# Optimization experiments

Hardware: AMD Instinct MI355X
Metric: run time of the kernel (lower is better)

The kernel has to match this reference:

```python
import jax, jax.numpy as jnp
import numpy as np

B, S, D, H, DK, DFF, L = 4, 1024, 1024, 16, 64, 4096, 128

def setup_inputs() -> dict:
    key = jax.random.key(0)
    ks = jax.random.split(key, 20)
    stdv = 1.0 / np.sqrt(D)
    u = lambda k, shape, s=stdv: jax.random.uniform(k, shape, jnp.float32, -s, s)
    x = jax.random.normal(ks[0], (B, S, D), jnp.float32)
    causal = jnp.triu(jnp.ones((S, S), bool), 1)          # True = masked
    attn_mask = jnp.broadcast_to(causal, (B, S, S))
    return {
        "x": x,
        "attn_mask": attn_mask,
        "W_q": u(ks[1], (H * DK, D)), "b_q": jnp.zeros((H * DK,)),
        "W_k": u(ks[2], (H * DK, D)), "b_k": jnp.zeros((H * DK,)),
        "W_v": u(ks[3], (H * DK, D)), "b_v": jnp.zeros((H * DK,)),
        "W_o": u(ks[4], (D, H * DK)), "b_o": jnp.zeros((D,)),
        "W_rel": u(ks[5], (2 * L + 1, DK), 1.0 / np.sqrt(DK)),
        "ln1_alpha": jnp.ones((D,)), "ln1_bias": jnp.zeros((D,)),
        "ln2_alpha": jnp.ones((D,)), "ln2_bias": jnp.zeros((D,)),
        "W1": u(ks[6], (DFF, D)), "b1": jnp.zeros((DFF,)),
        "W2": u(ks[7], (D, DFF)), "b2": jnp.zeros((D,)),
    }

def _layer_norm(x, alpha, bias, eps=1e-5):
    # Faithful to source: (x - mean) / (std + eps), std is biased (unbiased=False)
    m = jnp.mean(x, axis=-1, keepdims=True)
    std = jnp.sqrt(jnp.mean((x - m) ** 2, axis=-1, keepdims=True))
    return alpha * (x - m) / (std + eps) + bias

def reference(x, attn_mask, W_q, b_q, W_k, b_k, W_v, b_v, W_o, b_o, W_rel,
              ln1_alpha, ln1_bias, ln2_alpha, ln2_bias, W1, b1, W2, b2):
    b, s, d = x.shape
    q = (x @ W_q.T + b_q).reshape(b, s, H, DK)
    k = (x @ W_k.T + b_k).reshape(b, s, H, DK)
    v = (x @ W_v.T + b_v).reshape(b, s, H, DK)
    # relative position bias table lookup -> [s, s, DK]
    idx = jnp.clip(jnp.arange(s)[:, None] - jnp.arange(s)[None, :], -L, L) + L
    pos = W_rel[idx]
    # NOTE: original uses rel_pos_k_emb for BOTH pos_key and pos_value (as in source).
    scores = jnp.einsum('bqnd,bknd->bnqk', q, k) + jnp.einsum('bqnd,qkd->bnqk', q, pos)
    scores = scores / np.sqrt(DK)
    scores = jnp.where(attn_mask[:, None, :, :], jnp.float32(-10000.0), scores)
    attn = jax.nn.softmax(scores, axis=-1)
    out = jnp.einsum('bnqk,bknd->bnqd', attn, v) + jnp.einsum('bnqk,qkd->bnqd', attn, pos)
    out = out.transpose(0, 2, 1, 3).reshape(b, s, H * DK)
    out = out @ W_o.T + b_o
    # post-LN transformer layer: LN(x + attn), then LN(h + FFN(h))
    h = _layer_norm(x + out, ln1_alpha, ln1_bias)
    f = jax.nn.relu(h @ W1.T + b1) @ W2.T + b2
    return _layer_norm(h + f, ln2_alpha, ln2_bias)
```

## Files before the change

### kernel.cpp

```cpp
#include <hip/hip_runtime.h>
#include <cmath>
#include <cstdint>

typedef __bf16 bf16;
typedef __bf16 bf16x8 __attribute__((ext_vector_type(8)));
typedef __bf16 bf16x4 __attribute__((ext_vector_type(4)));
typedef float f32x4 __attribute__((ext_vector_type(4)));

__device__ __forceinline__ void async_ld16(const void* g, void* l) {
  __builtin_amdgcn_global_load_lds(
      (__attribute__((address_space(1))) void*)(uintptr_t)g,
      (__attribute__((address_space(3))) void*)l, 16, 0, 0);
}

__global__ __launch_bounds__(256) void cast_all(
    const float* __restrict__ x,  const float* __restrict__ wq, const float* __restrict__ wk,
    const float* __restrict__ wv, const float* __restrict__ wo, const float* __restrict__ w1,
    const float* __restrict__ w2,
    bf16* xb, bf16* wqb, bf16* wkb, bf16* wvb, bf16* wob, bf16* w1b, bf16* w2b)
{
  int i = blockIdx.x * 256 + threadIdx.x;
  const int M1 = 1 << 20, Q = 1 << 18;
  const float* src; bf16* dst; int off;
  if      (i < M1)            { src = x;  dst = xb;  off = i; }
  else if (i < M1 + Q)        { src = wq; dst = wqb; off = i - M1; }
  else if (i < M1 + 2 * Q)    { src = wk; dst = wkb; off = i - M1 - Q; }
  else if (i < M1 + 3 * Q)    { src = wv; dst = wvb; off = i - M1 - 2 * Q; }
  else if (i < M1 + 4 * Q)    { src = wo; dst = wob; off = i - M1 - 3 * Q; }
  else if (i < 3 * M1)        { src = w1; dst = w1b; off = i - M1 - 4 * Q; }
  else                        { src = w2; dst = w2b; off = i - 3 * M1; }
  float4 v = ((const float4*)src)[off];
  bf16x4 o; o[0]=(bf16)v.x; o[1]=(bf16)v.y; o[2]=(bf16)v.z; o[3]=(bf16)v.w;
  ((bf16x4*)dst)[off] = o;
}

template<int BM>
__device__ __forceinline__ void gemm_core(
    const bf16* __restrict__ A, const bf16* __restrict__ Bm, const float* __restrict__ bias,
    float* __restrict__ outF, bf16* __restrict__ outB,
    const float* __restrict__ residF, const bf16* __restrict__ residB,
    int N, int kld, int kbeg, int kend, int relu, bf16* As, bf16* Bs)
{
  constexpr int MI = BM / 32;
  const int tid  = threadIdx.x;
  const int wave = tid >> 6, lane = tid & 63;
  const int lr = lane & 15, lq = lane >> 4;
  const int bm = blockIdx.x * BM, bn = blockIdx.y * 128;
  const int wm = (wave >> 1) * (BM / 2), wn = (wave & 1) * 64;
  const int srow = lane >> 2, scol = (lane & 3) * 8;

  const f32x4 fz = {0.f, 0.f, 0.f, 0.f};
  f32x4 acc[MI][4];
#pragma unroll
  for (int i = 0; i < MI; i++)
#pragma unroll
    for (int j = 0; j < 4; j++) acc[i][j] = fz;

  for (int k0 = kbeg; k0 < kend; k0 += 32) {
    __syncthreads();
    if (BM == 128) {
#pragma unroll
      for (int cc = 0; cc < 2; ++cc) {
        int c = wave * 2 + cc;
        async_ld16(A + (size_t)(bm + c * 16 + srow) * kld + k0 + scol, As + c * 512);
      }
    } else {
      async_ld16(A + (size_t)(bm + wave * 16 + srow) * kld + k0 + scol, As + wave * 512);
    }
#pragma unroll
    for (int cc = 0; cc < 2; ++cc) {
      int c = wave * 2 + cc;
      async_ld16(Bm + (size_t)(bn + c * 16 + srow) * kld + k0 + scol, Bs + c * 512);
    }
    __syncthreads();
    bf16x8 af[MI], bfr[4];
#pragma unroll
    for (int mi = 0; mi < MI; mi++) af[mi]  = *(const bf16x8*)(As + (wm + mi*16 + lr)*32 + lq*8);
#pragma unroll
    for (int ni = 0; ni < 4; ni++) bfr[ni] = *(const bf16x8*)(Bs + (wn + ni*16 + lr)*32 + lq*8);
#pragma unroll
    for (int mi = 0; mi < MI; mi++)
#pragma unroll
      for (int ni = 0; ni < 4; ni++)
        acc[mi][ni] = __builtin_amdgcn_mfma_f32_16x16x32_bf16(af[mi], bfr[ni], acc[mi][ni], 0, 0, 0);
  }

#pragma unroll
  for (int ni = 0; ni < 4; ni++) {
    int n = bn + wn + ni*16 + lr;
    float bv = bias ? bias[n] : 0.0f;
#pragma unroll
    for (int mi = 0; mi < MI; mi++) {
#pragma unroll
      for (int r = 0; r < 4; r++) {
        int m = bm + wm + mi*16 + lq*4 + r;
        size_t idx = (size_t)m * N + n;
        float v = acc[mi][ni][r] + bv;
        if (relu) v = fmaxf(v, 0.0f);
        if (residF) v += residF[idx];
        if (residB) v += (float)residB[idx];
        if (outF) outF[idx] = v;
        else      outB[idx] = (bf16)v;
      }
    }
  }
}

template<int BM>
__global__ __launch_bounds__(256) void gemm_bt(
    const bf16* A, const bf16* Bm, const float* bias,
    float* outF, bf16* outB, const float* residF, const bf16* residB,
    int N, int K, int relu)
{
  __shared__ bf16 As[BM * 32];
  __shared__ bf16 Bs[128 * 32];
  gemm_core<BM>(A, Bm, bias, outF, outB, residF, residB, N, K, 0, K, relu, As, Bs);
}

__global__ __launch_bounds__(256) void gemm_splitk(
    const bf16* A, const bf16* Bm, float* part, int N, int kld, int kchunk)
{
  __shared__ bf16 As[128 * 32];
  __shared__ bf16 Bs[128 * 32];
  const int z = blockIdx.z;
  gemm_core<128>(A, Bm, nullptr, part + (size_t)z * 4096 * N, nullptr, nullptr, nullptr,
                 N, kld, z * kchunk, (z + 1) * kchunk, 0, As, Bs);
}

__global__ __launch_bounds__(256) void gemm_qkv(
    const bf16* A, const bf16* Bq, const bf16* Bk, const bf16* Bv,
    const float* bq, const float* bk, const float* bv,
    bf16* Oq, bf16* Ok, bf16* Ov, int N, int K)
{
  __shared__ bf16 As[128 * 32];
  __shared__ bf16 Bs[128 * 32];
  const bf16* Bm  = blockIdx.z == 0 ? Bq : (blockIdx.z == 1 ? Bk : Bv);
  const float* bi = blockIdx.z == 0 ? bq : (blockIdx.z == 1 ? bk : bv);
  bf16* O         = blockIdx.z == 0 ? Oq : (blockIdx.z == 1 ? Ok : Ov);
  gemm_core<128>(A, Bm, bi, nullptr, O, nullptr, nullptr, N, K, 0, K, 0, As, Bs);
}

#define S_LEN 1024
#define ROWSTR 1024

__global__ __launch_bounds__(256, 3) void attn_kernel(
    const bf16* __restrict__ Qg, const bf16* __restrict__ Kg, const bf16* __restrict__ Vg,
    const float* __restrict__ Wrel, bf16* __restrict__ Og)
{
  __shared__ __align__(16) bf16 hist[64][136];
  __shared__ __align__(16) bf16 rel_s[64][132];
  __shared__ __align__(16) bf16 vtp[9216];
  bf16* V_T  = vtp;
  bf16* Pb   = vtp + 4608;
  bf16* Wst  = vtp;
  bf16* Wr_t = vtp;
  float* lbuf = (float*)rel_s;
  float* hbuf = lbuf + 256;

  const int tid = threadIdx.x;
  const int wave = tid >> 6, lane = tid & 63;
  const int lr = lane & 15, lq = lane >> 4;
  const int qblk = 15 - blockIdx.x;
  const int b = blockIdx.y >> 4, h = blockIdx.y & 15;
  const int q0 = qblk * 64;
  const int T = qblk + 1;
  const int nearStart = (T > 3) ? T - 3 : 0;
  const size_t rowbase = (size_t)b * S_LEN * ROWSTR + h * 64;
  const f32x4 fz = {0.f, 0.f, 0.f, 0.f};

  for (int e = tid; e < 128 * 64; e += 256) {
    int t = e >> 6, d = e & 63;
    Wst[t * 72 + d] = (bf16)Wrel[(size_t)(128 + t) * 64 + d];
  }
  for (int e = tid; e < 64 * 68; e += 256) ((uint*)hist)[e] = 0u;

  bf16x8 qf[4][2];
#pragma unroll
  for (int qt = 0; qt < 4; qt++)
#pragma unroll
    for (int c = 0; c < 2; c++)
      qf[qt][c] = *(const bf16x8*)(Qg + rowbase + (size_t)(q0 + qt*16 + lr) * ROWSTR + c*32 + lq*8);

  bf16x8 wb[2];
#pragma unroll
  for (int c = 0; c < 2; c++)
#pragma unroll
    for (int j = 0; j < 8; j++)
      wb[c][j] = (bf16)Wrel[(size_t)256 * 64 + c*32 + lq*8 + j];

  __syncthreads();

#pragma unroll
  for (int tt = 0; tt < 2; ++tt)
#pragma unroll
    for (int qt = 0; qt < 4; ++qt) {
      f32x4 a = fz;
#pragma unroll
      for (int c = 0; c < 2; c++) {
        bf16x8 wf = *(const bf16x8*)(Wst + (wave*32 + tt*16 + lr) * 72 + c*32 + lq*8);
        a = __builtin_amdgcn_mfma_f32_16x16x32_bf16(wf, qf[qt][c], a, 0, 0, 0);
      }
      bf16x4 pk; pk[0]=(bf16)a[0]; pk[1]=(bf16)a[1]; pk[2]=(bf16)a[2]; pk[3]=(bf16)a[3];
      *(bf16x4*)(&rel_s[qt*16 + lr][wave*32 + tt*16 + lq*4]) = pk;
    }
  {
    f32x4 a = fz;
#pragma unroll
    for (int c = 0; c < 2; c++)
      a = __builtin_amdgcn_mfma_f32_16x16x32_bf16(wb[c], qf[wave][c], a, 0, 0, 0);
    if (lq == 0) rel_s[wave*16 + lr][128] = (bf16)a[0];
  }
  __syncthreads();

  float relc[4];
#pragma unroll
  for (int qt = 0; qt < 4; qt++) relc[qt] = 0.125f * (float)rel_s[qt*16 + lr][128];

  float l_p[4] = {0.f,0.f,0.f,0.f}, h_p[4] = {0.f,0.f,0.f,0.f};
  f32x4 acc_o[4];
#pragma unroll
  for (int dt = 0; dt < 4; dt++) acc_o[dt] = fz;

  const int vrow = 2 * (tid >> 3);
  const int vcol = (tid & 7) * 8;
  const int krow = 16 * wave + lr;

  uint4 va, vb, va2, vb2;
  bf16x8 kf0, kf1, kn0, kn1;
  {
    const bf16* vp = Vg + rowbase + (size_t)vrow * ROWSTR + vcol;
    va = *(const uint4*)vp; vb = *(const uint4*)(vp + ROWSTR);
    const bf16* kp = Kg + rowbase + (size_t)krow * ROWSTR + lq*8;
    kf0 = *(const bf16x8*)kp; kf1 = *(const bf16x8*)(kp + 32);
  }

  for (int kt = 0; kt < T; ++kt) {
    const int k0 = kt * 64;

    f32x4 sc[4];
#pragma unroll
    for (int qt = 0; qt < 4; qt++) {
      sc[qt] = __builtin_amdgcn_mfma_f32_16x16x32_bf16(kf0, qf[qt][0], fz, 0, 0, 0);
      sc[qt] = __builtin_amdgcn_mfma_f32_16x16x32_bf16(kf1, qf[qt][1], sc[qt], 0, 0, 0);
    }
    if (kt + 1 < T) {
      const bf16* vp = Vg + rowbase + (size_t)(k0 + 64 + vrow) * ROWSTR + vcol;
      va2 = *(const uint4*)vp; vb2 = *(const uint4*)(vp + ROWSTR);
      const bf16* kp = Kg + rowbase + (size_t)(k0 + 64 + krow) * ROWSTR + lq*8;
      kn0 = *(const bf16x8*)kp; kn1 = *(const bf16x8*)(kp + 32);
    }

    float pw[4][4];
    if (kt < nearStart) {
#pragma unroll
      for (int qt = 0; qt < 4; qt++) {
#pragma unroll
        for (int r = 0; r < 4; r++) pw[qt][r] = __expf(fmaf(sc[qt][r], 0.125f, relc[qt]));
        float s4 = pw[qt][0] + pw[qt][1] + pw[qt][2] + pw[qt][3];
        l_p[qt] += s4; h_p[qt] += s4;
      }
    } else {
#pragma unroll
      for (int qt = 0; qt < 4; qt++) {
        int qg = q0 + qt*16 + lr;
#pragma unroll
        for (int r = 0; r < 4; r++) {
          int kg = k0 + 16*wave + lq*4 + r;
          float p = 0.0f;
          if (kg <= qg) {
            int t = qg - kg; int tc = t > 128 ? 128 : t;
            p = __expf((sc[qt][r] + (float)rel_s[qt*16 + lr][tc]) * 0.125f);
            l_p[qt] += p;
            if (t >= 128) h_p[qt] += p;
            else          hist[qt*16 + lr][t] = (bf16)p;
          }
          pw[qt][r] = p;
        }
      }
    }

    __syncthreads();
    {
      const ushort* pa = (const ushort*)&va;
      const ushort* pb = (const ushort*)&vb;
#pragma unroll
      for (int j = 0; j < 8; j++) {
        uint w = (uint)pa[j] | ((uint)pb[j] << 16);
        *(uint*)(V_T + (vcol + j) * 72 + vrow) = w;
      }
    }
#pragma unroll
    for (int qt = 0; qt < 4; qt++) {
      bf16x4 pk; pk[0]=(bf16)pw[qt][0]; pk[1]=(bf16)pw[qt][1];
                 pk[2]=(bf16)pw[qt][2]; pk[3]=(bf16)pw[qt][3];
      *(bf16x4*)(Pb + (qt*16 + lr) * 72 + 16*wave + lq*4) = pk;
    }
    __syncthreads();

#pragma unroll
    for (int c = 0; c < 2; c++) {
      bf16x8 pf = *(const bf16x8*)(Pb + (16*wave + lr) * 72 + c*32 + lq*8);
#pragma unroll
      for (int dt = 0; dt < 4; dt++) {
        bf16x8 vf = *(const bf16x8*)(V_T + (dt*16 + lr) * 72 + c*32 + lq*8);
        acc_o[dt] = __builtin_amdgcn_mfma_f32_16x16x32_bf16(pf, vf, acc_o[dt], 0, 0, 0);
      }
    }
    kf0 = kn0; kf1 = kn1; va = va2; vb = vb2;
  }

#pragma unroll
  for (int qt = 0; qt < 4; qt++) {
    l_p[qt] += __shfl_xor(l_p[qt], 16); l_p[qt] += __shfl_xor(l_p[qt], 32);
    h_p[qt] += __shfl_xor(h_p[qt], 16); h_p[qt] += __shfl_xor(h_p[qt], 32);
  }
  __syncthreads();
  if (lq == 0) {
#pragma unroll
    for (int qt = 0; qt < 4; qt++) {
      lbuf[wave*64 + qt*16 + lr] = l_p[qt];
      hbuf[wave*64 + qt*16 + lr] = h_p[qt];
    }
  }
  for (int e = tid; e < 64 * 128; e += 256) {
    int d = e >> 7, t = e & 127;
    Wr_t[d * 136 + t] = (bf16)Wrel[(size_t)(128 + t) * 64 + d];
  }
  __syncthreads();
#pragma unroll
  for (int c = 0; c < 4; c++) {
    bf16x8 hf = *(const bf16x8*)&hist[wave*16 + lr][c*32 + lq*8];
#pragma unroll
    for (int dt = 0; dt < 4; dt++) {
      bf16x8 wf = *(const bf16x8*)(Wr_t + (dt*16 + lr) * 136 + c*32 + lq*8);
      acc_o[dt] = __builtin_amdgcn_mfma_f32_16x16x32_bf16(hf, wf, acc_o[dt], 0, 0, 0);
    }
  }
  float l4[4], h4[4];
#pragma unroll
  for (int r = 0; r < 4; r++) {
    int q = wave*16 + lq*4 + r;
    l4[r] = lbuf[q] + lbuf[64+q] + lbuf[128+q] + lbuf[192+q];
    h4[r] = hbuf[q] + hbuf[64+q] + hbuf[128+q] + hbuf[192+q];
  }
#pragma unroll
  for (int dt = 0; dt < 4; dt++) {
    float wv = Wrel[(size_t)256 * 64 + dt*16 + lr];
#pragma unroll
    for (int r = 0; r < 4; r++) acc_o[dt][r] += h4[r] * wv;
  }
#pragma unroll
  for (int dt = 0; dt < 4; dt++)
#pragma unroll
    for (int r = 0; r < 4; r++) {
      int qg = q0 + wave*16 + lq*4 + r;
      Og[rowbase + (size_t)qg * ROWSTR + dt*16 + lr] = (bf16)(acc_o[dt][r] / l4[r]);
    }
}

__global__ __launch_bounds__(256) void ln_fuse(
    const float* __restrict__ pA, const float* __restrict__ pB,
    const float* __restrict__ bias,
    const float* __restrict__ residF, const bf16* __restrict__ residB,
    const float* __restrict__ alpha, const float* __restrict__ beta,
    float* __restrict__ outF, bf16* __restrict__ outB)
{
  const int row = blockIdx.x, tid = threadIdx.x;
  const int lane = tid & 63, wave = tid >> 6;
  const size_t base = (size_t)row * 1024;
  float4 v = ((const float4*)(pA + base))[tid];
  float4 v2 = ((const float4*)(pB + base))[tid];
  v.x += v2.x; v.y += v2.y; v.z += v2.z; v.w += v2.w;
  float4 bv = ((const float4*)bias)[tid];
  v.x += bv.x; v.y += bv.y; v.z += bv.z; v.w += bv.w;
  if (residF) {
    float4 rv = ((const float4*)(residF + base))[tid];
    v.x += rv.x; v.y += rv.y; v.z += rv.z; v.w += rv.w;
  }
  if (residB) {
    bf16x4 rv = ((const bf16x4*)(residB + base))[tid];
    v.x += (float)rv[0]; v.y += (float)rv[1]; v.z += (float)rv[2]; v.w += (float)rv[3];
  }
  float s  = v.x + v.y + v.z + v.w;
  float ss = v.x*v.x + v.y*v.y + v.z*v.z + v.w*v.w;
#pragma unroll
  for (int off = 32; off; off >>= 1) { s += __shfl_down(s, off); ss += __shfl_down(ss, off); }
  __shared__ float rs[4], rss[4];
  if (lane == 0) { rs[wave] = s; rss[wave] = ss; }
  __syncthreads();
  s  = rs[0] + rs[1] + rs[2] + rs[3];
  ss = rss[0] + rss[1] + rss[2] + rss[3];
  float mean = s * (1.0f / 1024.0f);
  float var  = ss * (1.0f / 1024.0f) - mean * mean;
  float inv  = 1.0f / (sqrtf(fmaxf(var, 0.0f)) + 1e-5f);
  float4 a = ((const float4*)alpha)[tid];
  float4 bb = ((const float4*)beta)[tid];
  float o0 = a.x * (v.x - mean) * inv + bb.x;
  float o1 = a.y * (v.y - mean) * inv + bb.y;
  float o2 = a.z * (v.z - mean) * inv + bb.z;
  float o3 = a.w * (v.w - mean) * inv + bb.w;
  if (outF) { float4 o = {o0, o1, o2, o3}; ((float4*)(outF + base))[tid] = o; }
  if (outB) { bf16x4 o; o[0]=(bf16)o0; o[1]=(bf16)o1; o[2]=(bf16)o2; o[3]=(bf16)o3;
              ((bf16x4*)(outB + base))[tid] = o; }
}

extern "C" void kernel_launch(void* const* d_in, const int* in_sizes, int n_in,
                              void* d_out, int out_size, void* d_ws, size_t ws_size,
                              hipStream_t stream) {
  (void)in_sizes; (void)n_in; (void)out_size; (void)ws_size;
  const int D = 1024, DFF = 4096;

  const float* x    = (const float*)d_in[0];
  const float* Wq   = (const float*)d_in[2];
  const float* bq   = (const float*)d_in[3];
  const float* Wk   = (const float*)d_in[4];
  const float* bk   = (const float*)d_in[5];
  const float* Wv   = (const float*)d_in[6];
  const float* bv   = (const float*)d_in[7];
  const float* Wo   = (const float*)d_in[8];
  const float* bo   = (const float*)d_in[9];
  const float* Wrel = (const float*)d_in[10];
  const float* g1   = (const float*)d_in[11];
  const float* be1  = (const float*)d_in[12];
  const float* g2   = (const float*)d_in[13];
  const float* be2  = (const float*)d_in[14];
  const float* W1   = (const float*)d_in[15];
  const float* b1   = (const float*)d_in[16];
  const float* W2   = (const float*)d_in[17];
  const float* b2   = (const float*)d_in[18];

  char* ws = (char*)d_ws;
  const size_t MB = 1024 * 1024;
  bf16*  xb   = (bf16*)(ws + 0);
  bf16*  Wqb  = (bf16*)(ws + 8  * MB);
  bf16*  Wkb  = (bf16*)(ws + 10 * MB);
  bf16*  Wvb  = (bf16*)(ws + 12 * MB);
  bf16*  Wob  = (bf16*)(ws + 14 * MB);
  bf16*  W1b  = (bf16*)(ws + 16 * MB);
  bf16*  W2b  = (bf16*)(ws + 24 * MB);
  bf16*  Qb   = (bf16*)(ws + 32 * MB);
  bf16*  Kb   = (bf16*)(ws + 40 * MB);
  bf16*  Vb   = (bf16*)(ws + 48 * MB);
  bf16*  AOb  = (bf16*)(ws + 56 * MB);
  float* part = (float*)(ws + 64 * MB);
  bf16*  f1   = Qb;
  bf16*  hb   = xb;

  cast_all<<<16384, 256, 0, stream>>>(x, Wq, Wk, Wv, Wo, W1, W2,
                                      xb, Wqb, Wkb, Wvb, Wob, W1b, W2b);

  gemm_qkv<<<dim3(32, 8, 3), 256, 0, stream>>>(xb, Wqb, Wkb, Wvb, bq, bk, bv, Qb, Kb, Vb, D, D);
  attn_kernel<<<dim3(16, 64), 256, 0, stream>>>(Qb, Kb, Vb, Wrel, AOb);
  gemm_splitk<<<dim3(32, 8, 2), 256, 0, stream>>>(AOb, Wob, part, D, D, 512);
  ln_fuse<<<4096, 256, 0, stream>>>(part, part + 4096 * 1024, bo, x, nullptr, g1, be1, nullptr, hb);
  gemm_bt<128><<<dim3(32, 32), 256, 0, stream>>>(hb, W1b, b1, nullptr, f1, nullptr, nullptr, DFF, D, 1);
  gemm_splitk<<<dim3(32, 8, 2), 256, 0, stream>>>(f1, W2b, part, D, DFF, 2048);
  ln_fuse<<<4096, 256, 0, stream>>>(part, part + 4096 * 1024, b2, nullptr, hb, g2, be2, (float*)d_out, nullptr);
}
```

Before: 414.8 us.

## Double-buffer GEMM LDS tiles, pre-transpose V, and fold softmax scale into exp2

The shared GEMM core now uses two LDS buffers for A and B. The next K-slice's async global-to-LDS loads are issued right after the barrier, so they overlap the current slice's MFMAs and each iteration needs one barrier instead of two. A new transpose_v kernel writes V head-major and transposed, so the attention kernel can store V tiles into LDS with vector stores under an XOR swizzle instead of a per-element scatter. The softmax scale and log2(e) are folded into the relative-position scores so exp2f can replace __expf. The costs are an extra launch plus a V round trip through memory, twice the GEMM LDS footprint, and dropping the attention kernel's min-blocks occupancy hint.

```diff
diff --git a/kernel.cpp b/kernel.cpp
--- a/kernel.cpp
+++ b/kernel.cpp
@@ -6,6 +6,8 @@
 typedef __bf16 bf16x8 __attribute__((ext_vector_type(8)));
 typedef __bf16 bf16x4 __attribute__((ext_vector_type(4)));
 typedef float f32x4 __attribute__((ext_vector_type(4)));
+
+#define CEXP 0.1803368852f
 
 __device__ __forceinline__ void async_ld16(const void* g, void* l) {
   __builtin_amdgcn_global_load_lds(
@@ -56,28 +58,37 @@
 #pragma unroll
     for (int j = 0; j < 4; j++) acc[i][j] = fz;
 
-  for (int k0 = kbeg; k0 < kend; k0 += 32) {
-    __syncthreads();
+  auto issue = [&](int k0, int buf) {
+    bf16* Ad = As + buf * (BM * 32);
+    bf16* Bd = Bs + buf * (128 * 32);
     if (BM == 128) {
 #pragma unroll
       for (int cc = 0; cc < 2; ++cc) {
         int c = wave * 2 + cc;
-        async_ld16(A + (size_t)(bm + c * 16 + srow) * kld + k0 + scol, As + c * 512);
+        async_ld16(A + (size_t)(bm + c * 16 + srow) * kld + k0 + scol, Ad + c * 512);
       }
     } else {
-      async_ld16(A + (size_t)(bm + wave * 16 + srow) * kld + k0 + scol, As + wave * 512);
+      async_ld16(A + (size_t)(bm + wave * 16 + srow) * kld + k0 + scol, Ad + wave * 512);
     }
 #pragma unroll
     for (int cc = 0; cc < 2; ++cc) {
       int c = wave * 2 + cc;
-      async_ld16(Bm + (size_t)(bn + c * 16 + srow) * kld + k0 + scol, Bs + c * 512);
-    }
+      async_ld16(Bm + (size_t)(bn + c * 16 + srow) * kld + k0 + scol, Bd + c * 512);
+    }
+  };
+
+  const int nit = (kend - kbeg) >> 5;
+  issue(kbeg, 0);
+  for (int i = 0; i < nit; i++) {
     __syncthreads();
+    if (i + 1 < nit) issue(kbeg + (i + 1) * 32, (i + 1) & 1);
+    const bf16* Ab = As + (i & 1) * (BM * 32);
+    const bf16* Bb = Bs + (i & 1) * (128 * 32);
     bf16x8 af[MI], bfr[4];
 #pragma unroll
-    for (int mi = 0; mi < MI; mi++) af[mi]  = *(const bf16x8*)(As + (wm + mi*16 + lr)*32 + lq*8);
-#pragma unroll
-    for (int ni = 0; ni < 4; ni++) bfr[ni] = *(const bf16x8*)(Bs + (wn + ni*16 + lr)*32 + lq*8);
+    for (int mi = 0; mi < MI; mi++) af[mi]  = *(const bf16x8*)(Ab + (wm + mi*16 + lr)*32 + lq*8);
+#pragma unroll
+    for (int ni = 0; ni < 4; ni++) bfr[ni] = *(const bf16x8*)(Bb + (wn + ni*16 + lr)*32 + lq*8);
 #pragma unroll
     for (int mi = 0; mi < MI; mi++)
 #pragma unroll
@@ -112,16 +123,16 @@
     float* outF, bf16* outB, const float* residF, const bf16* residB,
     int N, int K, int relu)
 {
-  __shared__ bf16 As[BM * 32];
-  __shared__ bf16 Bs[128 * 32];
+  __shared__ bf16 As[2 * BM * 32];
+  __shared__ bf16 Bs[2 * 128 * 32];
   gemm_core<BM>(A, Bm, bias, outF, outB, residF, residB, N, K, 0, K, relu, As, Bs);
 }
 
 __global__ __launch_bounds__(256) void gemm_splitk(
     const bf16* A, const bf16* Bm, float* part, int N, int kld, int kchunk)
 {
-  __shared__ bf16 As[128 * 32];
-  __shared__ bf16 Bs[128 * 32];
+  __shared__ bf16 As[2 * 128 * 32];
+  __shared__ bf16 Bs[2 * 128 * 32];
   const int z = blockIdx.z;
   gemm_core<128>(A, Bm, nullptr, part + (size_t)z * 4096 * N, nullptr, nullptr, nullptr,
                  N, kld, z * kchunk, (z + 1) * kchunk, 0, As, Bs);
@@ -132,28 +143,50 @@
     const float* bq, const float* bk, const float* bv,
     bf16* Oq, bf16* Ok, bf16* Ov, int N, int K)
 {
-  __shared__ bf16 As[128 * 32];
-  __shared__ bf16 Bs[128 * 32];
+  __shared__ bf16 As[2 * 128 * 32];
+  __shared__ bf16 Bs[2 * 128 * 32];
   const bf16* Bm  = blockIdx.z == 0 ? Bq : (blockIdx.z == 1 ? Bk : Bv);
   const float* bi = blockIdx.z == 0 ? bq : (blockIdx.z == 1 ? bk : bv);
   bf16* O         = blockIdx.z == 0 ? Oq : (blockIdx.z == 1 ? Ok : Ov);
   gemm_core<128>(A, Bm, bi, nullptr, O, nullptr, nullptr, N, K, 0, K, 0, As, Bs);
 }
 
+__global__ __launch_bounds__(256) void transpose_v(const bf16* __restrict__ V, bf16* __restrict__ Vt) {
+  __shared__ bf16 t[64][72];
+  const int tid = threadIdx.x;
+  const int sblk = blockIdx.x;
+  const int bh = blockIdx.y;
+  const int b = bh >> 4, h = bh & 15;
+  const int sr = tid >> 2, dc = (tid & 3) * 16;
+  const bf16* src = V + ((size_t)(b * 1024 + sblk * 64 + sr)) * 1024 + h * 64 + dc;
+  bf16x8 r0 = *(const bf16x8*)src;
+  bf16x8 r1 = *(const bf16x8*)(src + 8);
+  *(bf16x8*)(&t[sr][dc]) = r0;
+  *(bf16x8*)(&t[sr][dc + 8]) = r1;
+  __syncthreads();
+  const int dr = tid >> 2, sc = (tid & 3) * 16;
+  bf16 o[16];
+#pragma unroll
+  for (int j = 0; j < 16; j++) o[j] = t[sc + j][dr];
+  bf16* dst = Vt + ((size_t)(bh * 64 + dr)) * 1024 + sblk * 64 + sc;
+  *(bf16x8*)dst = *(bf16x8*)&o[0];
+  *(bf16x8*)(dst + 8) = *(bf16x8*)&o[8];
+}
+
 #define S_LEN 1024
 #define ROWSTR 1024
 
-__global__ __launch_bounds__(256, 3) void attn_kernel(
-    const bf16* __restrict__ Qg, const bf16* __restrict__ Kg, const bf16* __restrict__ Vg,
+__global__ __launch_bounds__(256) void attn_kernel(
+    const bf16* __restrict__ Qg, const bf16* __restrict__ Kg, const bf16* __restrict__ Vt,
     const float* __restrict__ Wrel, bf16* __restrict__ Og)
 {
   __shared__ __align__(16) bf16 hist[64][136];
   __shared__ __align__(16) bf16 rel_s[64][132];
-  __shared__ __align__(16) bf16 vtp[9216];
-  bf16* V_T  = vtp;
-  bf16* Pb   = vtp + 4608;
-  bf16* Wst  = vtp;
-  bf16* Wr_t = vtp;
+  __shared__ __align__(16) bf16 ovl[8704];
+  bf16* V_T  = ovl;
+  bf16* Pb   = ovl + 4096;
+  bf16* Wst  = ovl;
+  bf16* Wr_t = ovl;
   float* lbuf = (float*)rel_s;
   float* hbuf = lbuf + 256;
 
@@ -161,17 +194,17 @@
   const int wave = tid >> 6, lane = tid & 63;
   const int lr = lane & 15, lq = lane >> 4;
   const int qblk = 15 - blockIdx.x;
-  const int b = blockIdx.y >> 4, h = blockIdx.y & 15;
+  const int bh = blockIdx.y;
+  const int b = bh >> 4, h = bh & 15;
   const int q0 = qblk * 64;
   const int T = qblk + 1;
   const int nearStart = (T > 3) ? T - 3 : 0;
   const size_t rowbase = (size_t)b * S_LEN * ROWSTR + h * 64;
+  const size_t vtbase = (size_t)(bh * 64) * 1024;
   const f32x4 fz = {0.f, 0.f, 0.f, 0.f};
 
-  for (int e = tid; e < 128 * 64; e += 256) {
-    int t = e >> 6, d = e & 63;
-    Wst[t * 72 + d] = (bf16)Wrel[(size_t)(128 + t) * 64 + d];
-  }
+  for (int e = tid; e < 128 * 64; e += 256)
+    Wst[e] = (bf16)Wrel[(size_t)(128 + (e >> 6)) * 64 + (e & 63)];
   for (int e = tid; e < 64 * 68; e += 256) ((uint*)hist)[e] = 0u;
 
   bf16x8 qf[4][2];
@@ -197,10 +230,11 @@
       f32x4 a = fz;
 #pragma unroll
       for (int c = 0; c < 2; c++) {
-        bf16x8 wf = *(const bf16x8*)(Wst + (wave*32 + tt*16 + lr) * 72 + c*32 + lq*8);
+        bf16x8 wf = *(const bf16x8*)(Wst + (wave*32 + tt*16 + lr) * 64 + c*32 + lq*8);
         a = __builtin_amdgcn_mfma_f32_16x16x32_bf16(wf, qf[qt][c], a, 0, 0, 0);
       }
-      bf16x4 pk; pk[0]=(bf16)a[0]; pk[1]=(bf16)a[1]; pk[2]=(bf16)a[2]; pk[3]=(bf16)a[3];
+      bf16x4 pk; pk[0]=(bf16)(a[0]*CEXP); pk[1]=(bf16)(a[1]*CEXP);
+                 pk[2]=(bf16)(a[2]*CEXP); pk[3]=(bf16)(a[3]*CEXP);
       *(bf16x4*)(&rel_s[qt*16 + lr][wave*32 + tt*16 + lq*4]) = pk;
     }
   {
@@ -208,28 +242,28 @@
 #pragma unroll
     for (int c = 0; c < 2; c++)
       a = __builtin_amdgcn_mfma_f32_16x16x32_bf16(wb[c], qf[wave][c], a, 0, 0, 0);
-    if (lq == 0) rel_s[wave*16 + lr][128] = (bf16)a[0];
+    if (lq == 0) rel_s[wave*16 + lr][128] = (bf16)(a[0]*CEXP);
   }
   __syncthreads();
 
   float relc[4];
 #pragma unroll
-  for (int qt = 0; qt < 4; qt++) relc[qt] = 0.125f * (float)rel_s[qt*16 + lr][128];
+  for (int qt = 0; qt < 4; qt++) relc[qt] = (float)rel_s[qt*16 + lr][128];
 
   float l_p[4] = {0.f,0.f,0.f,0.f}, h_p[4] = {0.f,0.f,0.f,0.f};
   f32x4 acc_o[4];
 #pragma unroll
   for (int dt = 0; dt < 4; dt++) acc_o[dt] = fz;
 
-  const int vrow = 2 * (tid >> 3);
-  const int vcol = (tid & 7) * 8;
+  const int vd1 = tid >> 3;
+  const int vj  = (tid & 7) ^ (vd1 & 7);
   const int krow = 16 * wave + lr;
 
   uint4 va, vb, va2, vb2;
   bf16x8 kf0, kf1, kn0, kn1;
   {
-    const bf16* vp = Vg + rowbase + (size_t)vrow * ROWSTR + vcol;
-    va = *(const uint4*)vp; vb = *(const uint4*)(vp + ROWSTR);
+    const bf16* vp = Vt + vtbase + (size_t)vd1 * 1024 + vj * 8;
+    va = *(const uint4*)vp; vb = *(const uint4*)(vp + 32 * 1024);
     const bf16* kp = Kg + rowbase + (size_t)krow * ROWSTR + lq*8;
     kf0 = *(const bf16x8*)kp; kf1 = *(const bf16x8*)(kp + 32);
   }
@@ -244,8 +278,8 @@
       sc[qt] = __builtin_amdgcn_mfma_f32_16x16x32_bf16(kf1, qf[qt][1], sc[qt], 0, 0, 0);
     }
     if (kt + 1 < T) {
-      const bf16* vp = Vg + rowbase + (size_t)(k0 + 64 + vrow) * ROWSTR + vcol;
-      va2 = *(const uint4*)vp; vb2 = *(const uint4*)(vp + ROWSTR);
+      const bf16* vp = Vt + vtbase + (size_t)vd1 * 1024 + k0 + 64 + vj * 8;
+      va2 = *(const uint4*)vp; vb2 = *(const uint4*)(vp + 32 * 1024);
       const bf16* kp = Kg + rowbase + (size_t)(k0 + 64 + krow) * ROWSTR + lq*8;
       kn0 = *(const bf16x8*)kp; kn1 = *(const bf16x8*)(kp + 32);
     }
@@ -255,7 +289,7 @@
 #pragma unroll
       for (int qt = 0; qt < 4; qt++) {
 #pragma unroll
-        for (int r = 0; r < 4; r++) pw[qt][r] = __expf(fmaf(sc[qt][r], 0.125f, relc[qt]));
+        for (int r = 0; r < 4; r++) pw[qt][r] = exp2f(fmaf(sc[qt][r], CEXP, relc[qt]));
         float s4 = pw[qt][0] + pw[qt][1] + pw[qt][2] + pw[qt][3];
         l_p[qt] += s4; h_p[qt] += s4;
       }
@@ -269,7 +303,7 @@
           float p = 0.0f;
           if (kg <= qg) {
             int t = qg - kg; int tc = t > 128 ? 128 : t;
-            p = __expf((sc[qt][r] + (float)rel_s[qt*16 + lr][tc]) * 0.125f);
+            p = exp2f(fmaf(sc[qt][r], CEXP, (float)rel_s[qt*16 + lr][tc]));
             l_p[qt] += p;
             if (t >= 128) h_p[qt] += p;
             else          hist[qt*16 + lr][t] = (bf16)p;
@@ -280,15 +314,8 @@
     }
 
     __syncthreads();
-    {
-      const ushort* pa = (const ushort*)&va;
-      const ushort* pb = (const ushort*)&vb;
-#pragma unroll
-      for (int j = 0; j < 8; j++) {
-        uint w = (uint)pa[j] | ((uint)pb[j] << 16);
-        *(uint*)(V_T + (vcol + j) * 72 + vrow) = w;
-      }
-    }
+    *(uint4*)(V_T + tid * 8) = va;
+    *(uint4*)(V_T + (tid + 256) * 8) = vb;
 #pragma unroll
     for (int qt = 0; qt < 4; qt++) {
       bf16x4 pk; pk[0]=(bf16)pw[qt][0]; pk[1]=(bf16)pw[qt][1];
@@ -302,7 +329,9 @@
       bf16x8 pf = *(const bf16x8*)(Pb + (16*wave + lr) * 72 + c*32 + lq*8);
 #pragma unroll
       for (int dt = 0; dt < 4; dt++) {
-        bf16x8 vf = *(const bf16x8*)(V_T + (dt*16 + lr) * 72 + c*32 + lq*8);
+        int vd = dt*16 + lr;
+        int jx = (c*4 + lq) ^ (vd & 7);
+        bf16x8 vf = *(const bf16x8*)(V_T + ((vd << 3) + jx) * 8);
         acc_o[dt] = __builtin_amdgcn_mfma_f32_16x16x32_bf16(pf, vf, acc_o[dt], 0, 0, 0);
       }
     }
@@ -441,7 +470,8 @@
   bf16*  Qb   = (bf16*)(ws + 32 * MB);
   bf16*  Kb   = (bf16*)(ws + 40 * MB);
   bf16*  Vb   = (bf16*)(ws + 48 * MB);
-  bf16*  AOb  = (bf16*)(ws + 56 * MB);
+  bf16*  Vt   = (bf16*)(ws + 56 * MB);
+  bf16*  AOb  = (bf16*)(ws + 48 * MB);
   float* part = (float*)(ws + 64 * MB);
   bf16*  f1   = Qb;
   bf16*  hb   = xb;
@@ -450,7 +480,8 @@
                                       xb, Wqb, Wkb, Wvb, Wob, W1b, W2b);
 
   gemm_qkv<<<dim3(32, 8, 3), 256, 0, stream>>>(xb, Wqb, Wkb, Wvb, bq, bk, bv, Qb, Kb, Vb, D, D);
-  attn_kernel<<<dim3(16, 64), 256, 0, stream>>>(Qb, Kb, Vb, Wrel, AOb);
+  transpose_v<<<dim3(16, 64), 256, 0, stream>>>(Vb, Vt);
+  attn_kernel<<<dim3(16, 64), 256, 0, stream>>>(Qb, Kb, Vt, Wrel, AOb);
   gemm_splitk<<<dim3(32, 8, 2), 256, 0, stream>>>(AOb, Wob, part, D, D, 512);
   ln_fuse<<<4096, 256, 0, stream>>>(part, part + 4096 * 1024, bo, x, nullptr, g1, be1, nullptr, hb);
   gemm_bt<128><<<dim3(32, 32), 256, 0, stream>>>(hb, W1b, b1, nullptr, f1, nullptr, nullptr, DFF, D, 1);
```

New measurement: 413.7 us. No clear change (-0.3%).
